# Optimization experiments

Measured on AMD Instinct MI355X. Metric: run time of the kernel, lower is better.

## Reference

```python
import jax, jax.numpy as jnp
import numpy as np

B, S, D, DK = 4, 2048, 1024, 1024


def setup_inputs() -> dict:
    key = jax.random.key(0)
    kx, kq, kk, kv = jax.random.split(key, 4)
    return {
        "x": jax.random.normal(kx, (B, S, D), dtype=jnp.float32),
        "WQ": jax.random.normal(kq, (D, DK), dtype=jnp.float32),
        "WK": jax.random.normal(kk, (D, DK), dtype=jnp.float32),
        "WV": jax.random.normal(kv, (D, DK), dtype=jnp.float32),
    }


def reference(x, WQ, WK, WV):
    # q,k,v: [B,S,DK]
    q = x @ WQ
    k = x @ WK
    v = x @ WV
    scale = 1.0 / np.sqrt(DK).astype(np.float32)
    scores = jnp.einsum("bqd,bkd->bqk", q, k) * scale  # [B,S,S]
    # NOTE: original uses nn.Softmax(dim=1) -> normalize over the QUERY axis (axis 1)
    attn = jax.nn.softmax(scores, axis=1)
    return jnp.einsum("bqk,bkd->bqd", attn, v)
```

## Files before the change

kernel.cpp:

```cpp
#include <hip/hip_runtime.h>

constexpr int Bc  = 4;
constexpr int Sc  = 2048;
constexpr int Dc  = 1024;
constexpr int DKc = 1024;
constexpr long BSc = (long)Bc * Sc;

typedef __attribute__((ext_vector_type(8))) __bf16 bf16x8;
typedef __attribute__((ext_vector_type(4))) __bf16 bf16x4;
typedef __attribute__((ext_vector_type(4))) float  floatx4;

__device__ inline __bf16 f2bf(float f) {
  unsigned u = __builtin_bit_cast(unsigned, f);
  u = (u + 0x7FFFu + ((u >> 16) & 1u)) >> 16;
  unsigned short s = (unsigned short)u;
  return __builtin_bit_cast(__bf16, s);
}
__device__ inline float bf2f(__bf16 h) {
  unsigned u = ((unsigned)__builtin_bit_cast(unsigned short, h)) << 16;
  return __builtin_bit_cast(float, u);
}

__device__ inline void stage16(const __bf16* g, __bf16* l) {
  __builtin_amdgcn_global_load_lds(
      (const __attribute__((address_space(1))) unsigned int*)g,
      (__attribute__((address_space(3))) unsigned int*)l, 16, 0, 0);
}

__device__ __forceinline__ void bar_raw() {
  asm volatile("" ::: "memory");
  __builtin_amdgcn_s_barrier();
  asm volatile("" ::: "memory");
}
template <int N>
__device__ __forceinline__ void vmwait() {
  asm volatile("s_waitcnt vmcnt(%0)" :: "n"(N));
  __builtin_amdgcn_sched_barrier(0);
}

__global__ __launch_bounds__(256) void prep(
    const float* __restrict__ x,  __bf16* __restrict__ xhi, __bf16* __restrict__ xlo,
    const float* __restrict__ wq, __bf16* __restrict__ qhi, __bf16* __restrict__ qlo,
    const float* __restrict__ wk, __bf16* __restrict__ khi, __bf16* __restrict__ klo,
    const float* __restrict__ wv, __bf16* __restrict__ vthi) {
  __shared__ float tile[32][33];
  long blk = blockIdx.x;
  if (blk >= 10240) {
    int t   = (int)(blk - 10240);
    int bx  = t & 31, by = t >> 5;
    int thx = threadIdx.x & 31, thy = threadIdx.x >> 5;
    int xI  = bx * 32 + thx, yI = by * 32 + thy;
#pragma unroll
    for (int j = 0; j < 32; j += 8)
      tile[thy + j][thx] = wv[(long)(yI + j) * DKc + xI];
    __syncthreads();
    int xO = by * 32 + thx, yO = bx * 32 + thy;
#pragma unroll
    for (int j = 0; j < 32; j += 8)
      vthi[(long)(yO + j) * Dc + xO] = f2bf(tile[thx][thy + j]);
    return;
  }
  const float* in; __bf16 *hi, *lo; long base;
  if (blk < 8192)      { in = x;  hi = xhi; lo = xlo; base = blk * 1024; }
  else if (blk < 9216) { in = wq; hi = qhi; lo = qlo; base = (blk - 8192) * 1024; }
  else                 { in = wk; hi = khi; lo = klo; base = (blk - 9216) * 1024; }
  long i = base + (long)threadIdx.x * 4;
  float4 f = *(const float4*)(in + i);
  __bf16 h0 = f2bf(f.x), h1 = f2bf(f.y), h2 = f2bf(f.z), h3 = f2bf(f.w);
  bf16x4 hv = {h0, h1, h2, h3};
  bf16x4 lv = {f2bf(f.x - bf2f(h0)), f2bf(f.y - bf2f(h1)),
               f2bf(f.z - bf2f(h2)), f2bf(f.w - bf2f(h3))};
  *(bf16x4*)(hi + i) = hv;
  *(bf16x4*)(lo + i) = lv;
}

struct SCtx {
  const __bf16 *pAh, *pAl, *pBh, *pBl;
  __bf16* lds;
  int stLds;
  int aoff, boff;
};

template <int WA, int WB, int WC, bool SAL, bool S2A, bool S2B>
__device__ __forceinline__ void tile_step(const SCtx& c, int t,
                                          floatx4 (&acc)[8][4]) {
  constexpr int K = 1024;
  constexpr int BH = 8192, BL = 16384, AL = 24576;
  __bf16* cur = c.lds + (t & 1) * 32768;
  __bf16* oth = c.lds + ((t & 1) ^ 1) * 32768;
  bf16x8 af[8], bfr[4];

  vmwait<WA>();
  bar_raw();
#pragma unroll
  for (int mt = 0; mt < 8; ++mt)
    af[mt] = *(const bf16x8*)(cur + c.aoff + mt * 512);
#pragma unroll
  for (int nt = 0; nt < 4; ++nt)
    bfr[nt] = *(const bf16x8*)(cur + BH + c.boff + nt * 512);
  if (SAL) {
    const __bf16* s = c.pAl + (t + 1) * 32;
    stage16(s, oth + AL + c.stLds);
    stage16(s + 16 * K, oth + AL + c.stLds + 512);
  }
  bar_raw();
  __builtin_amdgcn_s_setprio(1);
#pragma unroll
  for (int mt = 0; mt < 8; ++mt)
#pragma unroll
    for (int nt = 0; nt < 4; ++nt)
      acc[mt][nt] = __builtin_amdgcn_mfma_f32_16x16x32_bf16(af[mt], bfr[nt], acc[mt][nt], 0, 0, 0);
  __builtin_amdgcn_s_setprio(0);

  vmwait<WB>();
  bar_raw();
  {
    bf16x8 bfl[4];
#pragma unroll
    for (int nt = 0; nt < 4; ++nt)
      bfl[nt] = *(const bf16x8*)(cur + BL + c.boff + nt * 512);
    if (S2A) {
      const __bf16* sa = c.pAh + (t + 2) * 32;
      stage16(sa, cur + c.stLds);
      stage16(sa + 16 * K, cur + c.stLds + 512);
      stage16(c.pBh + (t + 2) * 32, cur + BH + c.stLds);
    }
    bar_raw();
    __builtin_amdgcn_s_setprio(1);
#pragma unroll
    for (int mt = 0; mt < 8; ++mt)
#pragma unroll
      for (int nt = 0; nt < 4; ++nt)
        acc[mt][nt] = __builtin_amdgcn_mfma_f32_16x16x32_bf16(af[mt], bfl[nt], acc[mt][nt], 0, 0, 0);
    __builtin_amdgcn_s_setprio(0);
  }

  vmwait<WC>();
  bar_raw();
  {
    bf16x8 afl[8];
#pragma unroll
    for (int mt = 0; mt < 8; ++mt)
      afl[mt] = *(const bf16x8*)(cur + AL + c.aoff + mt * 512);
    if (S2B) {
      stage16(c.pBh + (t + 2) * 32 + 16 * K, cur + BH + c.stLds + 512);
      const __bf16* sb = c.pBl + (t + 2) * 32;
      stage16(sb, cur + BL + c.stLds);
      stage16(sb + 16 * K, cur + BL + c.stLds + 512);
    }
    bar_raw();
    __builtin_amdgcn_s_setprio(1);
#pragma unroll
    for (int mt = 0; mt < 8; ++mt)
#pragma unroll
      for (int nt = 0; nt < 4; ++nt)
        acc[mt][nt] = __builtin_amdgcn_mfma_f32_16x16x32_bf16(afl[mt], bfr[nt], acc[mt][nt], 0, 0, 0);
    __builtin_amdgcn_s_setprio(0);
  }
}

__global__ __launch_bounds__(512, 2) void gemm_s2(
    const __bf16* __restrict__ thi, const __bf16* __restrict__ tlo,
    const __bf16* __restrict__ xhi, const __bf16* __restrict__ xlo,
    __bf16* __restrict__ P, float* __restrict__ Pmax, float* __restrict__ Psum) {
  __shared__ __align__(16) __bf16 smem[65536];
  constexpr int K = 1024;
  const int b    = blockIdx.z;
  const int m0   = blockIdx.y * 256;
  const int n0   = blockIdx.x * 256;
  const int wave = threadIdx.x >> 6;
  const int lane = threadIdx.x & 63;
  const int wm   = wave >> 2;
  const int wn   = wave & 3;
  const int sr   = lane >> 2;
  const int scol = ((lane & 3) ^ ((sr >> 1) & 3)) * 8;
  const int frow = lane & 15;
  const int pko  = ((lane >> 4) ^ ((frow >> 1) & 3)) * 8;

  SCtx c;
  const long batch = (long)Sc * 1024;
  const long ar = (long)(m0 + wave * 32 + sr) * K + scol;
  const long br = (long)(n0 + wave * 32 + sr) * K + scol;
  c.pAh = thi + (long)b * batch + ar;
  c.pAl = tlo + (long)b * batch + ar;
  c.pBh = xhi + (long)b * batch + br;
  c.pBl = xlo + (long)b * batch + br;
  c.lds = smem;
  c.stLds = wave * 1024;
  c.aoff = (wm * 128 + frow) * 32 + pko;
  c.boff = (wn * 64 + frow) * 32 + pko;

  {
    __bf16* b0 = smem;
    __bf16* b1 = smem + 32768;
    stage16(c.pAh, b0 + c.stLds);               stage16(c.pAh + 16 * K, b0 + c.stLds + 512);
    stage16(c.pBh, b0 + 8192 + c.stLds);        stage16(c.pBh + 16 * K, b0 + 8192 + c.stLds + 512);
    stage16(c.pBl, b0 + 16384 + c.stLds);       stage16(c.pBl + 16 * K, b0 + 16384 + c.stLds + 512);
    stage16(c.pAl, b0 + 24576 + c.stLds);       stage16(c.pAl + 16 * K, b0 + 24576 + c.stLds + 512);
    stage16(c.pAh + 32, b1 + c.stLds);          stage16(c.pAh + 32 + 16 * K, b1 + c.stLds + 512);
    stage16(c.pBh + 32, b1 + 8192 + c.stLds);   stage16(c.pBh + 32 + 16 * K, b1 + 8192 + c.stLds + 512);
    stage16(c.pBl + 32, b1 + 16384 + c.stLds);  stage16(c.pBl + 32 + 16 * K, b1 + 16384 + c.stLds + 512);
  }

  floatx4 acc[8][4];
  const floatx4 zero = {0.f, 0.f, 0.f, 0.f};
#pragma unroll
  for (int i = 0; i < 8; ++i)
#pragma unroll
    for (int j = 0; j < 4; ++j) acc[i][j] = zero;

#pragma unroll 1
  for (int t = 0; t < 30; ++t) tile_step<10, 10, 11, true, true, true>(c, t, acc);
  tile_step<10, 10, 8, true, false, false>(c, 30, acc);
  tile_step<4, 2, 0, false, false, false>(c, 31, acc);

  const int crow0 = (lane >> 4) * 4;
  const int ccol  = lane & 15;
  const int tid   = threadIdx.x;
  constexpr float scale = 0.03125f;
  float* smax = (float*)smem;
  float* ssum = smax + 512;

  float cm[4];
#pragma unroll
  for (int nt = 0; nt < 4; ++nt) {
    float mx = -3.0e38f;
#pragma unroll
    for (int mt = 0; mt < 8; ++mt)
#pragma unroll
      for (int r = 0; r < 4; ++r) mx = fmaxf(mx, acc[mt][nt][r] * scale);
    cm[nt] = mx;
  }
#pragma unroll
  for (int off = 16; off <= 32; off <<= 1)
#pragma unroll
    for (int nt = 0; nt < 4; ++nt)
      cm[nt] = fmaxf(cm[nt], __shfl_xor(cm[nt], off, 64));
  __syncthreads();
  if (lane < 16)
#pragma unroll
    for (int nt = 0; nt < 4; ++nt)
      smax[wm * 256 + wn * 64 + nt * 16 + lane] = cm[nt];
  __syncthreads();
  float mfin[4];
#pragma unroll
  for (int nt = 0; nt < 4; ++nt) {
    int cidx = wn * 64 + nt * 16 + ccol;
    mfin[nt] = fmaxf(smax[cidx], smax[256 + cidx]);
  }
  float ps[4];
#pragma unroll
  for (int nt = 0; nt < 4; ++nt) {
    float s = 0.f;
#pragma unroll
    for (int mt = 0; mt < 8; ++mt)
#pragma unroll
      for (int r = 0; r < 4; ++r)
        s += __expf(acc[mt][nt][r] * scale - mfin[nt]);
    ps[nt] = s;
  }
#pragma unroll
  for (int off = 16; off <= 32; off <<= 1)
#pragma unroll
    for (int nt = 0; nt < 4; ++nt) ps[nt] += __shfl_xor(ps[nt], off, 64);
  if (lane < 16)
#pragma unroll
    for (int nt = 0; nt < 4; ++nt)
      ssum[wm * 256 + wn * 64 + nt * 16 + lane] = ps[nt];
  __syncthreads();
  if (tid < 256) {
    long o = ((long)b * 8 + blockIdx.y) * Sc + n0 + tid;
    Pmax[o] = fmaxf(smax[tid], smax[256 + tid]);
    Psum[o] = ssum[tid] + ssum[256 + tid];
  }
  __syncthreads();
  __bf16* sT = smem;
#pragma unroll
  for (int nt = 0; nt < 4; ++nt) {
    int col = wn * 64 + nt * 16 + ccol;
#pragma unroll
    for (int mt = 0; mt < 8; ++mt) {
      int rowb = wm * 128 + mt * 16 + crow0;
#pragma unroll
      for (int r = 0; r < 4; ++r) {
        int row = rowb + r;
        sT[row * 256 + (col ^ (((row >> 2) & 3) << 4))] =
            f2bf(__expf(acc[mt][nt][r] * scale - mfin[nt]));
      }
    }
  }
  __syncthreads();
  __bf16* Pb = P + (long)b * ((long)Sc * Sc);
#pragma unroll
  for (int cc = 0; cc < 16; ++cc) {
    int flat = cc * 4096 + tid * 8;
    int row = flat >> 8, col = flat & 255;
    *(bf16x8*)(Pb + (long)(m0 + row) * Sc + n0 + col) =
        *(const bf16x8*)(sT + row * 256 + (col ^ (((row >> 2) & 3) << 4)));
  }
}

struct TCtx {
  const __bf16 *pAh, *pAl, *pBh, *pBl;
  __bf16* lds;
  int stA, stB;
  int aoff, boff;
};

template <int WA, int WB, int WC, bool SAL, bool S2AB, bool S2B>
__device__ __forceinline__ void tile_step_t(const TCtx& c, int t,
                                            floatx4 (&acc)[4][4]) {
  constexpr int K = 1024;
  constexpr int BH = 8192, BL = 12288, AL = 16384, BUF = 24576;
  __bf16* cur = c.lds + (t & 1) * BUF;
  __bf16* oth = c.lds + ((t & 1) ^ 1) * BUF;
  bf16x8 af[4], bfr[4];

  vmwait<WA>();
  bar_raw();
#pragma unroll
  for (int mt = 0; mt < 4; ++mt)
    af[mt] = *(const bf16x8*)(cur + c.aoff + mt * 512);
#pragma unroll
  for (int nt = 0; nt < 4; ++nt)
    bfr[nt] = *(const bf16x8*)(cur + BH + c.boff + nt * 512);
  if (SAL) {
    const __bf16* s = c.pAl + (t + 1) * 32;
    stage16(s, oth + AL + c.stA);
    stage16(s + 16 * K, oth + AL + c.stA + 512);
  }
  bar_raw();
  __builtin_amdgcn_s_setprio(1);
#pragma unroll
  for (int mt = 0; mt < 4; ++mt)
#pragma unroll
    for (int nt = 0; nt < 4; ++nt)
      acc[mt][nt] = __builtin_amdgcn_mfma_f32_16x16x32_bf16(af[mt], bfr[nt], acc[mt][nt], 0, 0, 0);
  __builtin_amdgcn_s_setprio(0);

  vmwait<WB>();
  bar_raw();
  {
    bf16x8 bfl[4];
#pragma unroll
    for (int nt = 0; nt < 4; ++nt)
      bfl[nt] = *(const bf16x8*)(cur + BL + c.boff + nt * 512);
    if (S2AB) {
      const __bf16* sa = c.pAh + (t + 2) * 32;
      stage16(sa, cur + c.stA);
      stage16(sa + 16 * K, cur + c.stA + 512);
      stage16(c.pBh + (t + 2) * 32, cur + BH + c.stB);
    }
    bar_raw();
    __builtin_amdgcn_s_setprio(1);
#pragma unroll
    for (int mt = 0; mt < 4; ++mt)
#pragma unroll
      for (int nt = 0; nt < 4; ++nt)
        acc[mt][nt] = __builtin_amdgcn_mfma_f32_16x16x32_bf16(af[mt], bfl[nt], acc[mt][nt], 0, 0, 0);
    __builtin_amdgcn_s_setprio(0);
  }

  vmwait<WC>();
  bar_raw();
  {
    bf16x8 afl[4];
#pragma unroll
    for (int mt = 0; mt < 4; ++mt)
      afl[mt] = *(const bf16x8*)(cur + AL + c.aoff + mt * 512);
    if (S2B) stage16(c.pBl + (t + 2) * 32, cur + BL + c.stB);
    bar_raw();
    __builtin_amdgcn_s_setprio(1);
#pragma unroll
    for (int mt = 0; mt < 4; ++mt)
#pragma unroll
      for (int nt = 0; nt < 4; ++nt)
        acc[mt][nt] = __builtin_amdgcn_mfma_f32_16x16x32_bf16(afl[mt], bfr[nt], acc[mt][nt], 0, 0, 0);
    __builtin_amdgcn_s_setprio(0);
  }
}

__global__ __launch_bounds__(512, 2) void gemm_t2(
    const __bf16* __restrict__ xhi, const __bf16* __restrict__ xlo,
    const __bf16* __restrict__ gthi, const __bf16* __restrict__ gtlo,
    __bf16* __restrict__ thi, __bf16* __restrict__ tlo) {
  __shared__ __align__(16) __bf16 smem[49152];
  constexpr int K = 1024;
  const int m0   = blockIdx.y * 256;
  const int n0   = blockIdx.x * 128;
  const int wave = threadIdx.x >> 6;
  const int lane = threadIdx.x & 63;
  const int wm   = wave >> 1;
  const int wn   = wave & 1;
  const int sr   = lane >> 2;
  const int scol = ((lane & 3) ^ ((sr >> 1) & 3)) * 8;
  const int frow = lane & 15;
  const int pko  = ((lane >> 4) ^ ((frow >> 1) & 3)) * 8;

  TCtx c;
  const long ar = (long)(m0 + wave * 32 + sr) * K + scol;
  const long br = (long)(n0 + wave * 16 + sr) * K + scol;
  c.pAh = xhi + ar;
  c.pAl = xlo + ar;
  c.pBh = gthi + br;
  c.pBl = gtlo + br;
  c.lds = smem;
  c.stA = wave * 1024;
  c.stB = wave * 512;
  c.aoff = (wm * 64 + frow) * 32 + pko;
  c.boff = (wn * 64 + frow) * 32 + pko;

  {
    __bf16* b0 = smem;
    __bf16* b1 = smem + 24576;
    stage16(c.pAh, b0 + c.stA);          stage16(c.pAh + 16 * K, b0 + c.stA + 512);
    stage16(c.pBh, b0 + 8192 + c.stB);
    stage16(c.pBl, b0 + 12288 + c.stB);
    stage16(c.pAl, b0 + 16384 + c.stA);  stage16(c.pAl + 16 * K, b0 + 16384 + c.stA + 512);
    stage16(c.pAh + 32, b1 + c.stA);     stage16(c.pAh + 32 + 16 * K, b1 + c.stA + 512);
    stage16(c.pBh + 32, b1 + 8192 + c.stB);
    stage16(c.pBl + 32, b1 + 12288 + c.stB);
  }

  floatx4 acc[4][4];
  const floatx4 zero = {0.f, 0.f, 0.f, 0.f};
#pragma unroll
  for (int i = 0; i < 4; ++i)
#pragma unroll
    for (int j = 0; j < 4; ++j) acc[i][j] = zero;

#pragma unroll 1
  for (int t = 0; t < 30; ++t) tile_step_t<7, 8, 9, true, true, true>(c, t, acc);
  tile_step_t<7, 8, 6, true, false, false>(c, 30, acc);
  tile_step_t<3, 2, 0, false, false, false>(c, 31, acc);

  const int crow0 = (lane >> 4) * 4;
  const int ccol  = lane & 15;
  const int tid   = threadIdx.x;
  __bf16* sT = smem;
#pragma unroll 1
  for (int pass = 0; pass < 2; ++pass) {
    __syncthreads();
#pragma unroll
    for (int nt = 0; nt < 4; ++nt) {
      int col = wn * 64 + nt * 16 + ccol;
#pragma unroll
      for (int mt = 0; mt < 4; ++mt) {
        int rowb = wm * 64 + mt * 16 + crow0;
#pragma unroll
        for (int r = 0; r < 4; ++r) {
          int row = rowb + r;
          float v = acc[mt][nt][r];
          __bf16 h = f2bf(v);
          sT[row * 128 + (col ^ (((row >> 2) & 3) << 4))] =
              pass ? f2bf(v - bf2f(h)) : h;
        }
      }
    }
    __syncthreads();
    __bf16* dst = pass ? tlo : thi;
#pragma unroll
    for (int cc = 0; cc < 8; ++cc) {
      int flat = cc * 4096 + tid * 8;
      int row = flat >> 7, col = flat & 127;
      *(bf16x8*)(dst + (long)(m0 + row) * DKc + n0 + col) =
          *(const bf16x8*)(sT + row * 128 + (col ^ (((row >> 2) & 3) << 4)));
    }
  }
}

struct PCtx {
  const __bf16 *pA, *pB;
  int stA, stB;
  int aoff, boff;
};

template <int KK, int WA, int WB, bool STG>
__device__ __forceinline__ void tile_step_pv(const PCtx& c, int t,
                                             __bf16* cur, __bf16* dst,
                                             floatx4 (&acc)[4][4]) {
  vmwait<WA>();
  bar_raw();
  {
    bf16x8 af[4], bfr[4];
#pragma unroll
    for (int mt = 0; mt < 4; ++mt)
      af[mt] = *(const bf16x8*)(cur + c.aoff + mt * 512);
#pragma unroll
    for (int nt = 0; nt < 4; ++nt)
      bfr[nt] = *(const bf16x8*)(cur + 16384 + c.boff + nt * 512);
    if (STG) {
      const __bf16* a = c.pA + (t + 2) * 64;
      stage16(a, dst + c.stA);
      stage16(a + 16 * KK, dst + c.stA + 512);
      stage16(c.pB + (t + 2) * 64, dst + 16384 + c.stB);
    }
    bar_raw();
    __builtin_amdgcn_s_setprio(1);
#pragma unroll
    for (int mt = 0; mt < 4; ++mt)
#pragma unroll
      for (int nt = 0; nt < 4; ++nt)
        acc[mt][nt] = __builtin_amdgcn_mfma_f32_16x16x32_bf16(af[mt], bfr[nt], acc[mt][nt], 0, 0, 0);
    __builtin_amdgcn_s_setprio(0);
  }
  vmwait<WB>();
  bar_raw();
  {
    bf16x8 af[4], bfr[4];
#pragma unroll
    for (int mt = 0; mt < 4; ++mt)
      af[mt] = *(const bf16x8*)(cur + 8192 + c.aoff + mt * 512);
#pragma unroll
    for (int nt = 0; nt < 4; ++nt)
      bfr[nt] = *(const bf16x8*)(cur + 20480 + c.boff + nt * 512);
    if (STG) {
      const __bf16* a = c.pA + (t + 2) * 64 + 32;
      stage16(a, dst + 8192 + c.stA);
      stage16(a + 16 * KK, dst + 8192 + c.stA + 512);
      stage16(c.pB + (t + 2) * 64 + 32, dst + 20480 + c.stB);
    }
    bar_raw();
    __builtin_amdgcn_s_setprio(1);
#pragma unroll
    for (int mt = 0; mt < 4; ++mt)
#pragma unroll
      for (int nt = 0; nt < 4; ++nt)
        acc[mt][nt] = __builtin_amdgcn_mfma_f32_16x16x32_bf16(af[mt], bfr[nt], acc[mt][nt], 0, 0, 0);
    __builtin_amdgcn_s_setprio(0);
  }
}

__global__ __launch_bounds__(256) void scale_p(__bf16* __restrict__ P,
                                               const float* __restrict__ ffac) {
  long i8 = (long)blockIdx.x * 256 + threadIdx.x;
  long base = i8 * 8;
  int k = (int)(base & (Sc - 1));
  int q = (int)((base >> 11) & (Sc - 1));
  int b = (int)(base >> 22);
  int t = q >> 8;
  const float* f = ffac + (((long)b * 8 + t) << 11) + k;
  float4 f0 = *(const float4*)f;
  float4 f1 = *(const float4*)(f + 4);
  bf16x8 p = *(const bf16x8*)(P + base);
  bf16x8 o;
  o[0] = f2bf(bf2f(p[0]) * f0.x);
  o[1] = f2bf(bf2f(p[1]) * f0.y);
  o[2] = f2bf(bf2f(p[2]) * f0.z);
  o[3] = f2bf(bf2f(p[3]) * f0.w);
  o[4] = f2bf(bf2f(p[4]) * f1.x);
  o[5] = f2bf(bf2f(p[5]) * f1.y);
  o[6] = f2bf(bf2f(p[6]) * f1.z);
  o[7] = f2bf(bf2f(p[7]) * f1.w);
  *(bf16x8*)(P + base) = o;
}

__global__ __launch_bounds__(512, 2) void gemm_pv2(
    const __bf16* __restrict__ P, const __bf16* __restrict__ vt,
    float* __restrict__ out) {
  __shared__ __align__(16) __bf16 smem[73728];
  constexpr int K = 2048;
  const int b    = blockIdx.z;
  const int m0   = blockIdx.x * 256;
  const int n0   = blockIdx.y * 128;
  const int wave = threadIdx.x >> 6;
  const int lane = threadIdx.x & 63;
  const int wm   = wave >> 1;
  const int wn   = wave & 1;
  const int sr   = lane >> 2;
  const int scol = ((lane & 3) ^ ((sr >> 1) & 3)) * 8;
  const int frow = lane & 15;
  const int pko  = ((lane >> 4) ^ ((frow >> 1) & 3)) * 8;

  PCtx c;
  c.pA = P + (long)b * Sc * Sc + (long)(m0 + wave * 32 + sr) * K + scol;
  c.pB = vt + (long)b * DKc * Sc + (long)(n0 + wave * 16 + sr) * K + scol;
  c.stA = wave * 1024;
  c.stB = wave * 512;
  c.aoff = (wm * 64 + frow) * 32 + pko;
  c.boff = (wn * 64 + frow) * 32 + pko;

  __bf16* B0 = smem;
  __bf16* B1 = smem + 24576;
  __bf16* B2 = smem + 49152;

  stage16(c.pA, B0 + c.stA);            stage16(c.pA + 16 * K, B0 + c.stA + 512);
  stage16(c.pB, B0 + 16384 + c.stB);
  stage16(c.pA + 32, B0 + 8192 + c.stA); stage16(c.pA + 32 + 16 * K, B0 + 8192 + c.stA + 512);
  stage16(c.pB + 32, B0 + 20480 + c.stB);
  stage16(c.pA + 64, B1 + c.stA);       stage16(c.pA + 64 + 16 * K, B1 + c.stA + 512);
  stage16(c.pB + 64, B1 + 16384 + c.stB);
  stage16(c.pA + 96, B1 + 8192 + c.stA); stage16(c.pA + 96 + 16 * K, B1 + 8192 + c.stA + 512);
  stage16(c.pB + 96, B1 + 20480 + c.stB);

  floatx4 acc[4][4];
  const floatx4 zero = {0.f, 0.f, 0.f, 0.f};
#pragma unroll
  for (int i = 0; i < 4; ++i)
#pragma unroll
    for (int j = 0; j < 4; ++j) acc[i][j] = zero;

#pragma unroll 1
  for (int t = 0; t < 30; t += 3) {
    tile_step_pv<2048, 9, 9, true>(c, t,     B0, B2, acc);
    tile_step_pv<2048, 9, 9, true>(c, t + 1, B1, B0, acc);
    tile_step_pv<2048, 9, 9, true>(c, t + 2, B2, B1, acc);
  }
  tile_step_pv<2048, 9, 6, false>(c, 30, B0, B0, acc);
  tile_step_pv<2048, 3, 0, false>(c, 31, B1, B1, acc);

  const int crow0 = (lane >> 4) * 4;
  const int ccol  = lane & 15;
#pragma unroll
  for (int nt = 0; nt < 4; ++nt) {
    int cn = n0 + wn * 64 + nt * 16 + ccol;
#pragma unroll
    for (int mt = 0; mt < 4; ++mt) {
#pragma unroll
      for (int r = 0; r < 4; ++r) {
        int cm_ = m0 + wm * 64 + mt * 16 + crow0 + r;
        out[(long)b * Sc * DKc + (long)cm_ * DKc + cn] = acc[mt][nt][r];
      }
    }
  }
}

constexpr int VSTR2 = 264;

__global__ __launch_bounds__(512, 2) void gemm_v2(
    const __bf16* __restrict__ xhi, const __bf16* __restrict__ wvthi,
    __bf16* __restrict__ vt) {
  __shared__ __align__(16) __bf16 smem[73728];
  constexpr int K = 1024;
  const int m0   = blockIdx.y * 256;
  const int n0   = blockIdx.x * 128;
  const int wave = threadIdx.x >> 6;
  const int lane = threadIdx.x & 63;
  const int wm   = wave >> 1;
  const int wn   = wave & 1;
  const int sr   = lane >> 2;
  const int scol = ((lane & 3) ^ ((sr >> 1) & 3)) * 8;
  const int frow = lane & 15;
  const int pko  = ((lane >> 4) ^ ((frow >> 1) & 3)) * 8;

  PCtx c;
  c.pA = xhi + (long)(m0 + wave * 32 + sr) * K + scol;
  c.pB = wvthi + (long)(n0 + wave * 16 + sr) * K + scol;
  c.stA = wave * 1024;
  c.stB = wave * 512;
  c.aoff = (wm * 64 + frow) * 32 + pko;
  c.boff = (wn * 64 + frow) * 32 + pko;

  __bf16* B0 = smem;
  __bf16* B1 = smem + 24576;
  __bf16* B2 = smem + 49152;

  stage16(c.pA, B0 + c.stA);            stage16(c.pA + 16 * K, B0 + c.stA + 512);
  stage16(c.pB, B0 + 16384 + c.stB);
  stage16(c.pA + 32, B0 + 8192 + c.stA); stage16(c.pA + 32 + 16 * K, B0 + 8192 + c.stA + 512);
  stage16(c.pB + 32, B0 + 20480 + c.stB);
  stage16(c.pA + 64, B1 + c.stA);       stage16(c.pA + 64 + 16 * K, B1 + c.stA + 512);
  stage16(c.pB + 64, B1 + 16384 + c.stB);
  stage16(c.pA + 96, B1 + 8192 + c.stA); stage16(c.pA + 96 + 16 * K, B1 + 8192 + c.stA + 512);
  stage16(c.pB + 96, B1 + 20480 + c.stB);

  floatx4 acc[4][4];
  const floatx4 zero = {0.f, 0.f, 0.f, 0.f};
#pragma unroll
  for (int i = 0; i < 4; ++i)
#pragma unroll
    for (int j = 0; j < 4; ++j) acc[i][j] = zero;

#pragma unroll 1
  for (int t = 0; t < 12; t += 3) {
    tile_step_pv<1024, 9, 9, true>(c, t,     B0, B2, acc);
    tile_step_pv<1024, 9, 9, true>(c, t + 1, B1, B0, acc);
    tile_step_pv<1024, 9, 9, true>(c, t + 2, B2, B1, acc);
  }
  tile_step_pv<1024, 9, 9, true >(c, 12, B0, B2, acc);
  tile_step_pv<1024, 9, 9, true >(c, 13, B1, B0, acc);
  tile_step_pv<1024, 9, 6, false>(c, 14, B2, B2, acc);
  tile_step_pv<1024, 3, 0, false>(c, 15, B0, B0, acc);

  const int crow0 = (lane >> 4) * 4;
  const int ccol  = lane & 15;
  const int tid   = threadIdx.x;
  __syncthreads();
  __bf16* sT = smem;
#pragma unroll
  for (int nt = 0; nt < 4; ++nt) {
    int nl = wn * 64 + nt * 16 + ccol;
#pragma unroll
    for (int mt = 0; mt < 4; ++mt) {
      int ml = wm * 64 + mt * 16 + crow0;
#pragma unroll
      for (int r = 0; r < 4; ++r)
        sT[(long)nl * VSTR2 + ml + r] = f2bf(acc[mt][nt][r]);
    }
  }
  __syncthreads();
  const int bb   = m0 >> 11;
  const int seq0 = m0 & (Sc - 1);
  __bf16* dst = vt + (long)bb * DKc * Sc + seq0;
#pragma unroll
  for (int cc = 0; cc < 8; ++cc) {
    int flat = cc * 4096 + tid * 8;
    int row = flat >> 8, col = flat & 255;
    *(bf16x8*)(dst + (long)(n0 + row) * Sc + col) =
        *(const bf16x8*)(sT + (long)row * VSTR2 + col);
  }
}

__global__ __launch_bounds__(256) void gemm_g64(
    const __bf16* __restrict__ Ahi, const __bf16* __restrict__ Alo,
    const __bf16* __restrict__ Bhi, const __bf16* __restrict__ Blo,
    __bf16* __restrict__ Chi, __bf16* __restrict__ Clo) {
  constexpr int K = Dc, N = DKc;
  __shared__ __align__(16) char smem[16384];
  __bf16* sAh = (__bf16*)smem;
  __bf16* sBh = sAh + 64 * 32;
  __bf16* sAl = sBh + 64 * 32;
  __bf16* sBl = sAl + 64 * 32;

  const int wave = threadIdx.x >> 6;
  const int lane = threadIdx.x & 63;
  const int wm   = wave >> 1, wn = wave & 1;
  const int m0   = blockIdx.y * 64;
  const int n0   = blockIdx.x * 64;

  const int sr   = lane >> 2;
  const int sc_  = lane & 3;
  const int scol = (sc_ ^ ((sr >> 1) & 3)) * 8;
  const int frow = lane & 15;
  const int pko  = ((lane >> 4) ^ ((frow >> 1) & 3)) * 8;

  floatx4 acc[2][2];
  const floatx4 zero = {0.f, 0.f, 0.f, 0.f};
#pragma unroll
  for (int i = 0; i < 2; ++i)
#pragma unroll
    for (int j = 0; j < 2; ++j) acc[i][j] = zero;

#pragma unroll 1
  for (int k0 = 0; k0 < K; k0 += 32) {
    const int rb = wave * 16;
    const long ga = (long)(m0 + rb + sr) * K + k0 + scol;
    const long gb = (long)(n0 + rb + sr) * K + k0 + scol;
    stage16(Ahi + ga, sAh + rb * 32);
    stage16(Alo + ga, sAl + rb * 32);
    stage16(Bhi + gb, sBh + rb * 32);
    stage16(Blo + gb, sBl + rb * 32);
    __syncthreads();

    bf16x8 af[2], bfr[2], afl[2], bfl[2];
#pragma unroll
    for (int t = 0; t < 2; ++t) {
      af[t]  = *(const bf16x8*)(sAh + (wm * 32 + t * 16 + frow) * 32 + pko);
      bfr[t] = *(const bf16x8*)(sBh + (wn * 32 + t * 16 + frow) * 32 + pko);
      afl[t] = *(const bf16x8*)(sAl + (wm * 32 + t * 16 + frow) * 32 + pko);
      bfl[t] = *(const bf16x8*)(sBl + (wn * 32 + t * 16 + frow) * 32 + pko);
    }
#pragma unroll
    for (int mt = 0; mt < 2; ++mt)
#pragma unroll
      for (int nt = 0; nt < 2; ++nt) {
        acc[mt][nt] = __builtin_amdgcn_mfma_f32_16x16x32_bf16(af[mt], bfr[nt], acc[mt][nt], 0, 0, 0);
        acc[mt][nt] = __builtin_amdgcn_mfma_f32_16x16x32_bf16(af[mt], bfl[nt], acc[mt][nt], 0, 0, 0);
        acc[mt][nt] = __builtin_amdgcn_mfma_f32_16x16x32_bf16(afl[mt], bfr[nt], acc[mt][nt], 0, 0, 0);
      }
    __syncthreads();
  }

  const int crow0 = (lane >> 4) * 4;
  const int ccol  = lane & 15;
  const int tid   = threadIdx.x;
  __bf16* sT = (__bf16*)smem;
#pragma unroll 1
  for (int pass = 0; pass < 2; ++pass) {
    __syncthreads();
#pragma unroll
    for (int nt = 0; nt < 2; ++nt) {
      int col = wn * 32 + nt * 16 + ccol;
#pragma unroll
      for (int mt = 0; mt < 2; ++mt) {
        int row = wm * 32 + mt * 16 + crow0;
#pragma unroll
        for (int r = 0; r < 4; ++r) {
          float v = acc[mt][nt][r];
          __bf16 h = f2bf(v);
          sT[(row + r) * 64 + col] = pass ? f2bf(v - bf2f(h)) : h;
        }
      }
    }
    __syncthreads();
    __bf16* dst = pass ? Clo : Chi;
#pragma unroll
    for (int c = 0; c < 2; ++c) {
      int flat = c * 2048 + tid * 8;
      int row = flat >> 6, col = flat & 63;
      *(bf16x8*)(dst + (long)(m0 + row) * N + n0 + col) = *(const bf16x8*)(sT + flat);
    }
  }
}

__global__ __launch_bounds__(256) void softmax_reduce(const float* __restrict__ Pmax,
                                                      const float* __restrict__ Psum,
                                                      float* __restrict__ Ffac) {
  int idx = blockIdx.x * 256 + threadIdx.x;
  int b = idx >> 11, k = idx & (Sc - 1);
  const float* pm = Pmax + (long)b * 8 * Sc + k;
  const float* ps = Psum + (long)b * 8 * Sc + k;
  float M = -3.0e38f;
#pragma unroll
  for (int t = 0; t < 8; ++t) M = fmaxf(M, pm[(long)t * Sc]);
  float S = 0.f;
#pragma unroll
  for (int t = 0; t < 8; ++t)
    S += ps[(long)t * Sc] * __expf(pm[(long)t * Sc] - M);
  float inv = 1.0f / S;
  float* fo = Ffac + (long)b * 8 * Sc + k;
#pragma unroll
  for (int t = 0; t < 8; ++t)
    fo[(long)t * Sc] = __expf(pm[(long)t * Sc] - M) * inv;
}

extern "C" void kernel_launch(void* const* d_in, const int* in_sizes, int n_in,
                              void* d_out, int out_size, void* d_ws, size_t ws_size,
                              hipStream_t stream) {
  const float* x  = (const float*)d_in[0];
  const float* WQ = (const float*)d_in[1];
  const float* WK = (const float*)d_in[2];
  const float* WV = (const float*)d_in[3];
  float* out = (float*)d_out;
  char* ws = (char*)d_ws;
  const long MB = 1024L * 1024L;

  __bf16* xhi  = (__bf16*)(ws + 0 * MB);
  __bf16* xlo  = (__bf16*)(ws + 16 * MB);
  __bf16* wqhi = (__bf16*)(ws + 32 * MB);
  __bf16* wqlo = (__bf16*)(ws + 34 * MB);
  __bf16* wkhi = (__bf16*)(ws + 36 * MB);
  __bf16* wklo = (__bf16*)(ws + 38 * MB);
  __bf16* wvthi= (__bf16*)(ws + 40 * MB);
  __bf16* gthi = (__bf16*)(ws + 44 * MB);
  __bf16* gtlo = (__bf16*)(ws + 46 * MB);
  __bf16* thi  = (__bf16*)(ws + 48 * MB);
  __bf16* tlo  = (__bf16*)(ws + 64 * MB);
  __bf16* vt   = (__bf16*)(ws + 80 * MB);
  __bf16* P    = (__bf16*)(ws + 96 * MB);
  float*  pmax = (float*)(ws + 128 * MB);
  float*  psum = (float*)(ws + 129 * MB);
  float*  ffac = (float*)(ws + 130 * MB);

  prep<<<11264, 256, 0, stream>>>(x, xhi, xlo, WQ, wqhi, wqlo, WK, wkhi, wklo,
                                  WV, wvthi);

  gemm_g64<<<dim3(16, 16), 256, 0, stream>>>(wkhi, wklo, wqhi, wqlo, gthi, gtlo);

  gemm_t2<<<dim3(DKc / 128, BSc / 256, 1), 512, 0, stream>>>(
      xhi, xlo, gthi, gtlo, thi, tlo);

  gemm_v2<<<dim3(DKc / 128, BSc / 256, 1), 512, 0, stream>>>(xhi, wvthi, vt);

  gemm_s2<<<dim3(Sc / 256, Sc / 256, Bc), 512, 0, stream>>>(
      thi, tlo, xhi, xlo, P, pmax, psum);

  softmax_reduce<<<32, 256, 0, stream>>>(pmax, psum, ffac);

  scale_p<<<8192, 256, 0, stream>>>(P, ffac);

  gemm_pv2<<<dim3(Sc / 256, DKc / 128, Bc), 512, 0, stream>>>(P, vt, out);
}
```

Baseline: 327.2 us.

## Hoist LDS fragment loads and collapse per-stage vmcnt waits into one per tile step

```diff
diff --git a/kernel.cpp b/kernel.cpp
--- a/kernel.cpp
+++ b/kernel.cpp
@@ -81,16 +81,16 @@
   int aoff, boff;
 };
 
-template <int WA, int WB, int WC, bool SAL, bool S2A, bool S2B>
+template <int W, bool SAL, bool S2A, bool S2B>
 __device__ __forceinline__ void tile_step(const SCtx& c, int t,
                                           floatx4 (&acc)[8][4]) {
   constexpr int K = 1024;
   constexpr int BH = 8192, BL = 16384, AL = 24576;
   __bf16* cur = c.lds + (t & 1) * 32768;
   __bf16* oth = c.lds + ((t & 1) ^ 1) * 32768;
-  bf16x8 af[8], bfr[4];
-
-  vmwait<WA>();
+  bf16x8 af[8], bfr[4], bfl[4];
+
+  vmwait<W>();
   bar_raw();
 #pragma unroll
   for (int mt = 0; mt < 8; ++mt)
@@ -98,12 +98,16 @@
 #pragma unroll
   for (int nt = 0; nt < 4; ++nt)
     bfr[nt] = *(const bf16x8*)(cur + BH + c.boff + nt * 512);
+#pragma unroll
+  for (int nt = 0; nt < 4; ++nt)
+    bfl[nt] = *(const bf16x8*)(cur + BL + c.boff + nt * 512);
   if (SAL) {
     const __bf16* s = c.pAl + (t + 1) * 32;
     stage16(s, oth + AL + c.stLds);
     stage16(s + 16 * K, oth + AL + c.stLds + 512);
   }
   bar_raw();
+
   __builtin_amdgcn_s_setprio(1);
 #pragma unroll
   for (int mt = 0; mt < 8; ++mt)
@@ -112,43 +116,33 @@
       acc[mt][nt] = __builtin_amdgcn_mfma_f32_16x16x32_bf16(af[mt], bfr[nt], acc[mt][nt], 0, 0, 0);
   __builtin_amdgcn_s_setprio(0);
 
-  vmwait<WB>();
+  bar_raw();
+  if (S2A) {
+    const __bf16* sa = c.pAh + (t + 2) * 32;
+    stage16(sa, cur + c.stLds);
+    stage16(sa + 16 * K, cur + c.stLds + 512);
+    stage16(c.pBh + (t + 2) * 32, cur + BH + c.stLds);
+  }
+  __builtin_amdgcn_s_setprio(1);
+#pragma unroll
+  for (int mt = 0; mt < 8; ++mt)
+#pragma unroll
+    for (int nt = 0; nt < 4; ++nt)
+      acc[mt][nt] = __builtin_amdgcn_mfma_f32_16x16x32_bf16(af[mt], bfl[nt], acc[mt][nt], 0, 0, 0);
+  __builtin_amdgcn_s_setprio(0);
+
   bar_raw();
   {
-    bf16x8 bfl[4];
-#pragma unroll
-    for (int nt = 0; nt < 4; ++nt)
-      bfl[nt] = *(const bf16x8*)(cur + BL + c.boff + nt * 512);
-    if (S2A) {
-      const __bf16* sa = c.pAh + (t + 2) * 32;
-      stage16(sa, cur + c.stLds);
-      stage16(sa + 16 * K, cur + c.stLds + 512);
-      stage16(c.pBh + (t + 2) * 32, cur + BH + c.stLds);
-    }
-    bar_raw();
-    __builtin_amdgcn_s_setprio(1);
-#pragma unroll
-    for (int mt = 0; mt < 8; ++mt)
-#pragma unroll
-      for (int nt = 0; nt < 4; ++nt)
-        acc[mt][nt] = __builtin_amdgcn_mfma_f32_16x16x32_bf16(af[mt], bfl[nt], acc[mt][nt], 0, 0, 0);
-    __builtin_amdgcn_s_setprio(0);
-  }
-
-  vmwait<WC>();
-  bar_raw();
-  {
-    bf16x8 afl[8];
-#pragma unroll
-    for (int mt = 0; mt < 8; ++mt)
-      afl[mt] = *(const bf16x8*)(cur + AL + c.aoff + mt * 512);
     if (S2B) {
       stage16(c.pBh + (t + 2) * 32 + 16 * K, cur + BH + c.stLds + 512);
       const __bf16* sb = c.pBl + (t + 2) * 32;
       stage16(sb, cur + BL + c.stLds);
       stage16(sb + 16 * K, cur + BL + c.stLds + 512);
     }
-    bar_raw();
+    bf16x8 afl[8];
+#pragma unroll
+    for (int mt = 0; mt < 8; ++mt)
+      afl[mt] = *(const bf16x8*)(cur + AL + c.aoff + mt * 512);
     __builtin_amdgcn_s_setprio(1);
 #pragma unroll
     for (int mt = 0; mt < 8; ++mt)
@@ -159,7 +153,7 @@
   }
 }
 
-__global__ __launch_bounds__(512, 2) void gemm_s2(
+__global__ __launch_bounds__(512, 2) void gemm_s4(
     const __bf16* __restrict__ thi, const __bf16* __restrict__ tlo,
     const __bf16* __restrict__ xhi, const __bf16* __restrict__ xlo,
     __bf16* __restrict__ P, float* __restrict__ Pmax, float* __restrict__ Psum) {
@@ -210,9 +204,9 @@
     for (int j = 0; j < 4; ++j) acc[i][j] = zero;
 
 #pragma unroll 1
-  for (int t = 0; t < 30; ++t) tile_step<10, 10, 11, true, true, true>(c, t, acc);
-  tile_step<10, 10, 8, true, false, false>(c, 30, acc);
-  tile_step<4, 2, 0, false, false, false>(c, 31, acc);
+  for (int t = 0; t < 30; ++t) tile_step<6, true, true, true>(c, t, acc);
+  tile_step<6, true, false, false>(c, 30, acc);
+  tile_step<0, false, false, false>(c, 31, acc);
 
   const int crow0 = (lane >> 4) * 4;
   const int ccol  = lane & 15;
@@ -307,16 +301,16 @@
   int aoff, boff;
 };
 
-template <int WA, int WB, int WC, bool SAL, bool S2AB, bool S2B>
+template <int W, bool SAL, bool S2AB, bool S2B>
 __device__ __forceinline__ void tile_step_t(const TCtx& c, int t,
                                             floatx4 (&acc)[4][4]) {
   constexpr int K = 1024;
   constexpr int BH = 8192, BL = 12288, AL = 16384, BUF = 24576;
   __bf16* cur = c.lds + (t & 1) * BUF;
   __bf16* oth = c.lds + ((t & 1) ^ 1) * BUF;
-  bf16x8 af[4], bfr[4];
-
-  vmwait<WA>();
+  bf16x8 af[4], bfr[4], bfl[4], afl[4];
+
+  vmwait<W>();
   bar_raw();
 #pragma unroll
   for (int mt = 0; mt < 4; ++mt)
@@ -324,12 +318,19 @@
 #pragma unroll
   for (int nt = 0; nt < 4; ++nt)
     bfr[nt] = *(const bf16x8*)(cur + BH + c.boff + nt * 512);
+#pragma unroll
+  for (int nt = 0; nt < 4; ++nt)
+    bfl[nt] = *(const bf16x8*)(cur + BL + c.boff + nt * 512);
+#pragma unroll
+  for (int mt = 0; mt < 4; ++mt)
+    afl[mt] = *(const bf16x8*)(cur + AL + c.aoff + mt * 512);
   if (SAL) {
     const __bf16* s = c.pAl + (t + 1) * 32;
     stage16(s, oth + AL + c.stA);
     stage16(s + 16 * K, oth + AL + c.stA + 512);
   }
   bar_raw();
+
   __builtin_amdgcn_s_setprio(1);
 #pragma unroll
   for (int mt = 0; mt < 4; ++mt)
@@ -338,49 +339,33 @@
       acc[mt][nt] = __builtin_amdgcn_mfma_f32_16x16x32_bf16(af[mt], bfr[nt], acc[mt][nt], 0, 0, 0);
   __builtin_amdgcn_s_setprio(0);
 
-  vmwait<WB>();
-  bar_raw();
-  {
-    bf16x8 bfl[4];
-#pragma unroll
-    for (int nt = 0; nt < 4; ++nt)
-      bfl[nt] = *(const bf16x8*)(cur + BL + c.boff + nt * 512);
-    if (S2AB) {
-      const __bf16* sa = c.pAh + (t + 2) * 32;
-      stage16(sa, cur + c.stA);
-      stage16(sa + 16 * K, cur + c.stA + 512);
-      stage16(c.pBh + (t + 2) * 32, cur + BH + c.stB);
-    }
-    bar_raw();
-    __builtin_amdgcn_s_setprio(1);
-#pragma unroll
-    for (int mt = 0; mt < 4; ++mt)
-#pragma unroll
-      for (int nt = 0; nt < 4; ++nt)
-        acc[mt][nt] = __builtin_amdgcn_mfma_f32_16x16x32_bf16(af[mt], bfl[nt], acc[mt][nt], 0, 0, 0);
-    __builtin_amdgcn_s_setprio(0);
-  }
-
-  vmwait<WC>();
-  bar_raw();
-  {
-    bf16x8 afl[4];
-#pragma unroll
-    for (int mt = 0; mt < 4; ++mt)
-      afl[mt] = *(const bf16x8*)(cur + AL + c.aoff + mt * 512);
-    if (S2B) stage16(c.pBl + (t + 2) * 32, cur + BL + c.stB);
-    bar_raw();
-    __builtin_amdgcn_s_setprio(1);
-#pragma unroll
-    for (int mt = 0; mt < 4; ++mt)
-#pragma unroll
-      for (int nt = 0; nt < 4; ++nt)
-        acc[mt][nt] = __builtin_amdgcn_mfma_f32_16x16x32_bf16(afl[mt], bfr[nt], acc[mt][nt], 0, 0, 0);
-    __builtin_amdgcn_s_setprio(0);
-  }
-}
-
-__global__ __launch_bounds__(512, 2) void gemm_t2(
+  bar_raw();
+  if (S2AB) {
+    const __bf16* sa = c.pAh + (t + 2) * 32;
+    stage16(sa, cur + c.stA);
+    stage16(sa + 16 * K, cur + c.stA + 512);
+    stage16(c.pBh + (t + 2) * 32, cur + BH + c.stB);
+  }
+  __builtin_amdgcn_s_setprio(1);
+#pragma unroll
+  for (int mt = 0; mt < 4; ++mt)
+#pragma unroll
+    for (int nt = 0; nt < 4; ++nt)
+      acc[mt][nt] = __builtin_amdgcn_mfma_f32_16x16x32_bf16(af[mt], bfl[nt], acc[mt][nt], 0, 0, 0);
+  __builtin_amdgcn_s_setprio(0);
+
+  bar_raw();
+  if (S2B) stage16(c.pBl + (t + 2) * 32, cur + BL + c.stB);
+  __builtin_amdgcn_s_setprio(1);
+#pragma unroll
+  for (int mt = 0; mt < 4; ++mt)
+#pragma unroll
+    for (int nt = 0; nt < 4; ++nt)
+      acc[mt][nt] = __builtin_amdgcn_mfma_f32_16x16x32_bf16(afl[mt], bfr[nt], acc[mt][nt], 0, 0, 0);
+  __builtin_amdgcn_s_setprio(0);
+}
+
+__global__ __launch_bounds__(512, 2) void gemm_t4(
     const __bf16* __restrict__ xhi, const __bf16* __restrict__ xlo,
     const __bf16* __restrict__ gthi, const __bf16* __restrict__ gtlo,
     __bf16* __restrict__ thi, __bf16* __restrict__ tlo) {
@@ -430,9 +415,9 @@
     for (int j = 0; j < 4; ++j) acc[i][j] = zero;
 
 #pragma unroll 1
-  for (int t = 0; t < 30; ++t) tile_step_t<7, 8, 9, true, true, true>(c, t, acc);
-  tile_step_t<7, 8, 6, true, false, false>(c, 30, acc);
-  tile_step_t<3, 2, 0, false, false, false>(c, 31, acc);
+  for (int t = 0; t < 30; ++t) tile_step_t<4, true, true, true>(c, t, acc);
+  tile_step_t<4, true, false, false>(c, 30, acc);
+  tile_step_t<0, false, false, false>(c, 31, acc);
 
   const int crow0 = (lane >> 4) * 4;
   const int ccol  = lane & 15;
@@ -475,60 +460,47 @@
   int aoff, boff;
 };
 
-template <int KK, int WA, int WB, bool STG>
+template <int KK, int W, bool STG>
 __device__ __forceinline__ void tile_step_pv(const PCtx& c, int t,
                                              __bf16* cur, __bf16* dst,
                                              floatx4 (&acc)[4][4]) {
-  vmwait<WA>();
-  bar_raw();
-  {
-    bf16x8 af[4], bfr[4];
-#pragma unroll
-    for (int mt = 0; mt < 4; ++mt)
-      af[mt] = *(const bf16x8*)(cur + c.aoff + mt * 512);
-#pragma unroll
-    for (int nt = 0; nt < 4; ++nt)
-      bfr[nt] = *(const bf16x8*)(cur + 16384 + c.boff + nt * 512);
-    if (STG) {
-      const __bf16* a = c.pA + (t + 2) * 64;
-      stage16(a, dst + c.stA);
-      stage16(a + 16 * KK, dst + c.stA + 512);
-      stage16(c.pB + (t + 2) * 64, dst + 16384 + c.stB);
-    }
-    bar_raw();
-    __builtin_amdgcn_s_setprio(1);
-#pragma unroll
-    for (int mt = 0; mt < 4; ++mt)
-#pragma unroll
-      for (int nt = 0; nt < 4; ++nt)
-        acc[mt][nt] = __builtin_amdgcn_mfma_f32_16x16x32_bf16(af[mt], bfr[nt], acc[mt][nt], 0, 0, 0);
-    __builtin_amdgcn_s_setprio(0);
-  }
-  vmwait<WB>();
-  bar_raw();
-  {
-    bf16x8 af[4], bfr[4];
-#pragma unroll
-    for (int mt = 0; mt < 4; ++mt)
-      af[mt] = *(const bf16x8*)(cur + 8192 + c.aoff + mt * 512);
-#pragma unroll
-    for (int nt = 0; nt < 4; ++nt)
-      bfr[nt] = *(const bf16x8*)(cur + 20480 + c.boff + nt * 512);
-    if (STG) {
-      const __bf16* a = c.pA + (t + 2) * 64 + 32;
-      stage16(a, dst + 8192 + c.stA);
-      stage16(a + 16 * KK, dst + 8192 + c.stA + 512);
-      stage16(c.pB + (t + 2) * 64 + 32, dst + 20480 + c.stB);
-    }
-    bar_raw();
-    __builtin_amdgcn_s_setprio(1);
-#pragma unroll
-    for (int mt = 0; mt < 4; ++mt)
-#pragma unroll
-      for (int nt = 0; nt < 4; ++nt)
-        acc[mt][nt] = __builtin_amdgcn_mfma_f32_16x16x32_bf16(af[mt], bfr[nt], acc[mt][nt], 0, 0, 0);
-    __builtin_amdgcn_s_setprio(0);
-  }
+  vmwait<W>();
+  bar_raw();
+  bf16x8 a0[4], b0[4], a1[4], b1[4];
+#pragma unroll
+  for (int mt = 0; mt < 4; ++mt)
+    a0[mt] = *(const bf16x8*)(cur + c.aoff + mt * 512);
+#pragma unroll
+  for (int nt = 0; nt < 4; ++nt)
+    b0[nt] = *(const bf16x8*)(cur + 16384 + c.boff + nt * 512);
+#pragma unroll
+  for (int mt = 0; mt < 4; ++mt)
+    a1[mt] = *(const bf16x8*)(cur + 8192 + c.aoff + mt * 512);
+#pragma unroll
+  for (int nt = 0; nt < 4; ++nt)
+    b1[nt] = *(const bf16x8*)(cur + 20480 + c.boff + nt * 512);
+  if (STG) {
+    const __bf16* a = c.pA + (t + 2) * 64;
+    stage16(a, dst + c.stA);
+    stage16(a + 16 * KK, dst + c.stA + 512);
+    stage16(c.pB + (t + 2) * 64, dst + 16384 + c.stB);
+    stage16(a + 32, dst + 8192 + c.stA);
+    stage16(a + 32 + 16 * KK, dst + 8192 + c.stA + 512);
+    stage16(c.pB + (t + 2) * 64 + 32, dst + 20480 + c.stB);
+  }
+  bar_raw();
+  __builtin_amdgcn_s_setprio(1);
+#pragma unroll
+  for (int mt = 0; mt < 4; ++mt)
+#pragma unroll
+    for (int nt = 0; nt < 4; ++nt)
+      acc[mt][nt] = __builtin_amdgcn_mfma_f32_16x16x32_bf16(a0[mt], b0[nt], acc[mt][nt], 0, 0, 0);
+#pragma unroll
+  for (int mt = 0; mt < 4; ++mt)
+#pragma unroll
+    for (int nt = 0; nt < 4; ++nt)
+      acc[mt][nt] = __builtin_amdgcn_mfma_f32_16x16x32_bf16(a1[mt], b1[nt], acc[mt][nt], 0, 0, 0);
+  __builtin_amdgcn_s_setprio(0);
 }
 
 __global__ __launch_bounds__(256) void scale_p(__bf16* __restrict__ P,
@@ -555,7 +527,7 @@
   *(bf16x8*)(P + base) = o;
 }
 
-__global__ __launch_bounds__(512, 2) void gemm_pv2(
+__global__ __launch_bounds__(512, 2) void gemm_pv3(
     const __bf16* __restrict__ P, const __bf16* __restrict__ vt,
     float* __restrict__ out) {
   __shared__ __align__(16) __bf16 smem[73728];
@@ -602,12 +574,12 @@
 
 #pragma unroll 1
   for (int t = 0; t < 30; t += 3) {
-    tile_step_pv<2048, 9, 9, true>(c, t,     B0, B2, acc);
-    tile_step_pv<2048, 9, 9, true>(c, t + 1, B1, B0, acc);
-    tile_step_pv<2048, 9, 9, true>(c, t + 2, B2, B1, acc);
-  }
-  tile_step_pv<2048, 9, 6, false>(c, 30, B0, B0, acc);
-  tile_step_pv<2048, 3, 0, false>(c, 31, B1, B1, acc);
+    tile_step_pv<2048, 6, true>(c, t,     B0, B2, acc);
+    tile_step_pv<2048, 6, true>(c, t + 1, B1, B0, acc);
+    tile_step_pv<2048, 6, true>(c, t + 2, B2, B1, acc);
+  }
+  tile_step_pv<2048, 6, false>(c, 30, B0, B0, acc);
+  tile_step_pv<2048, 0, false>(c, 31, B1, B1, acc);
 
   const int crow0 = (lane >> 4) * 4;
   const int ccol  = lane & 15;
@@ -627,7 +599,7 @@
 
 constexpr int VSTR2 = 264;
 
-__global__ __launch_bounds__(512, 2) void gemm_v2(
+__global__ __launch_bounds__(512, 2) void gemm_v3(
     const __bf16* __restrict__ xhi, const __bf16* __restrict__ wvthi,
     __bf16* __restrict__ vt) {
   __shared__ __align__(16) __bf16 smem[73728];
@@ -673,14 +645,14 @@
 
 #pragma unroll 1
   for (int t = 0; t < 12; t += 3) {
-    tile_step_pv<1024, 9, 9, true>(c, t,     B0, B2, acc);
-    tile_step_pv<1024, 9, 9, true>(c, t + 1, B1, B0, acc);
-    tile_step_pv<1024, 9, 9, true>(c, t + 2, B2, B1, acc);
-  }
-  tile_step_pv<1024, 9, 9, true >(c, 12, B0, B2, acc);
-  tile_step_pv<1024, 9, 9, true >(c, 13, B1, B0, acc);
-  tile_step_pv<1024, 9, 6, false>(c, 14, B2, B2, acc);
-  tile_step_pv<1024, 3, 0, false>(c, 15, B0, B0, acc);
+    tile_step_pv<1024, 6, true>(c, t,     B0, B2, acc);
+    tile_step_pv<1024, 6, true>(c, t + 1, B1, B0, acc);
+    tile_step_pv<1024, 6, true>(c, t + 2, B2, B1, acc);
+  }
+  tile_step_pv<1024, 6, true >(c, 12, B0, B2, acc);
+  tile_step_pv<1024, 6, true >(c, 13, B1, B0, acc);
+  tile_step_pv<1024, 6, false>(c, 14, B2, B2, acc);
+  tile_step_pv<1024, 0, false>(c, 15, B0, B0, acc);
 
   const int crow0 = (lane >> 4) * 4;
   const int ccol  = lane & 15;
@@ -857,17 +829,17 @@
 
   gemm_g64<<<dim3(16, 16), 256, 0, stream>>>(wkhi, wklo, wqhi, wqlo, gthi, gtlo);
 
-  gemm_t2<<<dim3(DKc / 128, BSc / 256, 1), 512, 0, stream>>>(
+  gemm_t4<<<dim3(DKc / 128, BSc / 256, 1), 512, 0, stream>>>(
       xhi, xlo, gthi, gtlo, thi, tlo);
 
-  gemm_v2<<<dim3(DKc / 128, BSc / 256, 1), 512, 0, stream>>>(xhi, wvthi, vt);
-
-  gemm_s2<<<dim3(Sc / 256, Sc / 256, Bc), 512, 0, stream>>>(
+  gemm_v3<<<dim3(DKc / 128, BSc / 256, 1), 512, 0, stream>>>(xhi, wvthi, vt);
+
+  gemm_s4<<<dim3(Sc / 256, Sc / 256, Bc), 512, 0, stream>>>(
       thi, tlo, xhi, xlo, P, pmax, psum);
 
   softmax_reduce<<<32, 256, 0, stream>>>(pmax, psum, ffac);
 
   scale_p<<<8192, 256, 0, stream>>>(P, ffac);
 
-  gemm_pv2<<<dim3(Sc / 256, DKc / 128, Bc), 512, 0, stream>>>(P, vt, out);
-}
+  gemm_pv3<<<dim3(Sc / 256, DKc / 128, Bc), 512, 0, stream>>>(P, vt, out);
+}
```

Measured after the change: 327.0 us. No clear change (-0.1%).
